# Kernel tuning notes

Hardware: AMD Instinct MI355X
Metric: run time of the kernel (lower is better)

Reference implementation:

```python
import jax, jax.numpy as jnp
import numpy as np

B, T, D = 8, 2048, 1024   # batch, seq_len (== block_size), n_embed
HS = 128                   # head_size

def setup_inputs() -> dict:
    key = jax.random.key(0)
    kx, kk, kq, kv = jax.random.split(key, 4)
    s = D ** -0.5  # torch Linear default init scale ~ U(-1/sqrt(in), 1/sqrt(in))
    x  = jax.random.normal(kx, (B, T, D), dtype=jnp.float32)
    Wk = jax.random.uniform(kk, (HS, D), jnp.float32, -s, s)
    Wq = jax.random.uniform(kq, (HS, D), jnp.float32, -s, s)
    Wv = jax.random.uniform(kv, (HS, D), jnp.float32, -s, s)
    return {"x": x, "Wk": Wk, "Wq": Wq, "Wv": Wv}

def reference(x, Wk, Wq, Wv):
    # single-head causal self-attention; dropout disabled (eval mode)
    Tlen = x.shape[1]
    k = jnp.einsum('btd,hd->bth', x, Wk)   # [B,T,HS]
    q = jnp.einsum('btd,hd->bth', x, Wq)
    v = jnp.einsum('btd,hd->bth', x, Wv)
    scale = Wk.shape[0] ** -0.5
    scores = jnp.einsum('bth,bsh->bts', q, k) * scale   # [B,T,T]
    causal = jnp.tril(jnp.ones((Tlen, Tlen), dtype=bool))
    scores = jnp.where(causal, scores, -jnp.inf)
    weights = jax.nn.softmax(scores, axis=-1)
    out = jnp.einsum('bts,bsh->bth', weights, v)        # [B,T,HS]
    return out
```

## Files before the change

kernel.cpp:

```cpp
#include <hip/hip_runtime.h>
#include <hip/hip_bf16.h>
#include <math.h>

#define BATCH_N 8
#define SEQ_T   2048
#define DIM_D   1024
#define HS_N    128

using bf16x8_t = __attribute__((ext_vector_type(8))) __bf16;
using bf16x4_t = __attribute__((ext_vector_type(4))) __bf16;
using f32x4_t  = __attribute__((ext_vector_type(4))) float;

__device__ __forceinline__ f32x4_t mfma_16x16x32(bf16x8_t a, bf16x8_t b, f32x4_t c) {
  return __builtin_amdgcn_mfma_f32_16x16x32_bf16(a, b, c, 0, 0, 0);
}

__device__ __forceinline__ void async_cp16(const void* g, void* l) {
  __builtin_amdgcn_global_load_lds(
      (const __attribute__((address_space(1))) unsigned int*)g,
      (__attribute__((address_space(3))) unsigned int*)l, 16, 0, 0);
}

#define BAR()      __builtin_amdgcn_s_barrier()
#define FENCE()    asm volatile("" ::: "memory")
#define WAIT_VM(n) asm volatile("s_waitcnt vmcnt(" #n ")" ::: "memory")
#define WAIT_LGKM0 asm volatile("s_waitcnt lgkmcnt(0)" ::: "memory")

__global__ __launch_bounds__(256) void castw_kernel(
    const float* __restrict__ Wk, const float* __restrict__ Wq,
    const float* __restrict__ Wv, __bf16* __restrict__ Wb,
    unsigned int* __restrict__ km) {
  if (blockIdx.x == 0 && threadIdx.x < 8) km[threadIdx.x] = 0u;
  int idx = blockIdx.x * 256 + threadIdx.x;
  int e   = idx * 4;
  int row = e >> 10;
  int col = e & 1023;
  const float* src;
  float sc = 1.0f;
  if (row < 128) {
    src = Wk + row * DIM_D + col;
  } else if (row < 256) {
    src = Wq + (row - 128) * DIM_D + col;
    sc  = 0.08838834764831845f;
  } else {
    src = Wv + (row - 256) * DIM_D + col;
  }
  float4 v = *(const float4*)src;
  bf16x4_t o;
  o[0] = (__bf16)(v.x * sc); o[1] = (__bf16)(v.y * sc);
  o[2] = (__bf16)(v.z * sc); o[3] = (__bf16)(v.w * sc);
  *(bf16x4_t*)(Wb + e) = o;
}

__global__ __launch_bounds__(256, 2) void proj_kernel(
    const float* __restrict__ x, const __bf16* __restrict__ Wb,
    __bf16* __restrict__ Qb, __bf16* __restrict__ Kb, __bf16* __restrict__ Vt) {
  __shared__ __align__(16) char psmem[81920];
  __bf16* A = (__bf16*)psmem;

  const int tid  = threadIdx.x;
  const int lane = tid & 63;
  const int wave = tid >> 6;
  const int lr = lane & 15;
  const int lq = lane >> 4;
  const int m0 = blockIdx.x * 32;

  f32x4_t acc[2][6];
  #pragma unroll
  for (int mt = 0; mt < 2; ++mt)
    #pragma unroll
    for (int nt = 0; nt < 6; ++nt) acc[mt][nt] = (f32x4_t){0.f, 0.f, 0.f, 0.f};

  auto stageB = [&](int bufi, int kt) {
    __bf16* Bs = (__bf16*)(psmem + 32768 + bufi * 24576);
    for (int c = wave; c < 24; c += 4) {
      const int row = c * 16 + (lane >> 2);
      const int u   = (lane & 3) ^ ((row >> 1) & 3);
      async_cp16(Wb + (size_t)row * DIM_D + kt * 32 + u * 8, Bs + c * 512);
    }
  };

  stageB(0, 0);

  for (int p = 0; p < 2; ++p) {
    __syncthreads();

    {
      const int r  = tid >> 3;
      const int t  = tid & 7;
      const float* xs = x + (size_t)(m0 + r) * DIM_D + p * 512;
      __bf16* as = A + r * 512;
      const int sw = r & 7;
      #pragma unroll
      for (int i = 0; i < 8; ++i) {
        const int u = t + 8 * i;
        float4 f0 = *(const float4*)(xs + u * 8);
        float4 f1 = *(const float4*)(xs + u * 8 + 4);
        bf16x8_t a;
        a[0] = (__bf16)f0.x; a[1] = (__bf16)f0.y;
        a[2] = (__bf16)f0.z; a[3] = (__bf16)f0.w;
        a[4] = (__bf16)f1.x; a[5] = (__bf16)f1.y;
        a[6] = (__bf16)f1.z; a[7] = (__bf16)f1.w;
        *(bf16x8_t*)(as + ((u ^ sw) * 8)) = a;
      }
    }
    __syncthreads();

    for (int kt2 = 0; kt2 < 16; ++kt2) {
      const int kt  = p * 16 + kt2;
      const int cur = kt & 1;
      if (kt + 1 < 32) {
        stageB(cur ^ 1, kt + 1);
        WAIT_VM(6);
      } else {
        WAIT_VM(0);
      }
      BAR();
      FENCE();
      const __bf16* Bs = (const __bf16*)(psmem + 32768 + cur * 24576);

      bf16x8_t af[2];
      #pragma unroll
      for (int mt = 0; mt < 2; ++mt) {
        const int ml = mt * 16 + lr;
        const int u  = kt2 * 4 + lq;
        af[mt] = *(const bf16x8_t*)(&A[ml * 512 + ((u ^ (ml & 7)) * 8)]);
      }
      bf16x8_t bfv[6];
      #pragma unroll
      for (int nt = 0; nt < 6; ++nt) {
        const int nl = wave * 96 + nt * 16 + lr;
        bfv[nt] = *(const bf16x8_t*)(&Bs[nl * 32 + ((lq ^ ((nl >> 1) & 3)) * 8)]);
      }
      #pragma unroll
      for (int mt = 0; mt < 2; ++mt)
        #pragma unroll
        for (int nt = 0; nt < 6; ++nt)
          acc[mt][nt] = mfma_16x16x32(af[mt], bfv[nt], acc[mt][nt]);
      WAIT_LGKM0;
      BAR();
      FENCE();
    }
  }

  #pragma unroll
  for (int mt = 0; mt < 2; ++mt) {
    const int t0 = m0 + mt * 16 + lq * 4;
    #pragma unroll
    for (int nt = 0; nt < 6; ++nt) {
      const int nn = wave * 96 + nt * 16 + lr;
      if (nn < 256) {
        __bf16* dst = (nn < 128) ? (Kb + nn) : (Qb + (nn - 128));
        #pragma unroll
        for (int r = 0; r < 4; ++r)
          dst[(size_t)(t0 + r) * HS_N] = (__bf16)acc[mt][nt][r];
      } else {
        const int bb = t0 >> 11;
        const int tl = t0 & 2047;
        bf16x4_t o;
        #pragma unroll
        for (int r = 0; r < 4; ++r) o[r] = (__bf16)acc[mt][nt][r];
        *(bf16x4_t*)(Vt + (size_t)bb * (HS_N * SEQ_T) + (size_t)(nn - 256) * SEQ_T + tl) = o;
      }
    }
  }
}

__global__ __launch_bounds__(256) void knorm_kernel(
    const __bf16* __restrict__ Kb, unsigned int* __restrict__ km) {
  const int t = blockIdx.x * 256 + threadIdx.x;
  const __bf16* kp = Kb + (size_t)t * HS_N;
  float ss = 0.f;
  #pragma unroll
  for (int i = 0; i < 16; ++i) {
    bf16x8_t v = *(const bf16x8_t*)(kp + i * 8);
    #pragma unroll
    for (int j = 0; j < 8; ++j) { float f = (float)v[j]; ss += f * f; }
  }
  #pragma unroll
  for (int off = 1; off < 64; off <<= 1) ss = fmaxf(ss, __shfl_xor(ss, off));
  if ((threadIdx.x & 63) == 0) atomicMax(km + (t >> 11), __float_as_uint(ss));
}

__global__ __launch_bounds__(256, 2) void attn_kernel(
    const __bf16* __restrict__ Qb, const __bf16* __restrict__ Kb,
    const __bf16* __restrict__ Vt, const unsigned int* __restrict__ km,
    __bf16* __restrict__ Opart, float* __restrict__ lpart) {
  __shared__ __align__(16) char smem[81920];
  __bf16* KsBase = (__bf16*)smem;
  __bf16* VsBase = (__bf16*)(smem + 32768);
  float*  Ofl    = (float*)smem;

  const int lane = threadIdx.x & 63;
  const int wave = threadIdx.x >> 6;
  const int lr = lane & 15;
  const int lq = lane >> 4;
  const int bid  = blockIdx.x;
  const int b    = bid & 7;
  const int rest = bid >> 3;
  const int jg   = 15 - (rest >> 2);
  const int p4   = rest & 3;
  const int Q0   = jg * 128;
  const int qa   = Q0 + wave * 32;
  const int ch   = 2 * (jg + 1);
  const int c0   = (p4 * ch) >> 2;
  const int c1   = ((p4 + 1) * ch) >> 2;

  const __bf16* Qbb = Qb + (size_t)b * (SEQ_T * HS_N);
  const __bf16* Kbb = Kb + (size_t)b * (SEQ_T * HS_N);
  const __bf16* Vbb = Vt + (size_t)b * (HS_N * SEQ_T);
  __bf16* pbA = (__bf16*)(smem + 65536 + wave * 4096);
  __bf16* pbB = (__bf16*)(smem + 65536 + wave * 4096 + 2048);

  bf16x8_t qf[2][4];
  #pragma unroll
  for (int t = 0; t < 2; ++t)
    #pragma unroll
    for (int ks = 0; ks < 4; ++ks)
      qf[t][ks] = *(const bf16x8_t*)(Qbb + (size_t)(qa + t * 16 + lr) * HS_N
                                     + ks * 32 + lq * 8);

  const float km2 = __uint_as_float(km[b]);
  float mrow[2][4];
  #pragma unroll
  for (int t = 0; t < 2; ++t) {
    float qn2 = 0.f;
    #pragma unroll
    for (int ks = 0; ks < 4; ++ks)
      #pragma unroll
      for (int j = 0; j < 8; ++j) { float f = (float)qf[t][ks][j]; qn2 += f * f; }
    qn2 += __shfl_xor(qn2, 16);
    qn2 += __shfl_xor(qn2, 32);
    #pragma unroll
    for (int r2 = 0; r2 < 4; ++r2)
      mrow[t][r2] = sqrtf(__shfl(qn2, lq * 4 + r2) * km2);
  }

  f32x4_t Oa[2][8];
  #pragma unroll
  for (int t = 0; t < 2; ++t)
    #pragma unroll
    for (int o = 0; o < 8; ++o) Oa[t][o] = (f32x4_t){0.f, 0.f, 0.f, 0.f};
  float lsum[2][4] = {{0.f,0.f,0.f,0.f},{0.f,0.f,0.f,0.f}};

  auto stage = [&](int bufi, int c) {
    const int kk = c * 64;
    __bf16* Ks = KsBase + bufi * 8192;
    for (int idx = wave; idx < 32; idx += 4) {
      if (idx < 16) {
        const int row = idx * 4 + (lane >> 4);
        const int u   = (lane & 15) ^ (row & 15);
        async_cp16(Kbb + (size_t)(kk + row) * HS_N + u * 8, Ks + idx * 512);
      } else {
        const int i2  = idx - 16;
        const int row = i2 * 8 + (lane >> 3);
        const int u   = (lane & 7) ^ (row & 7);
        async_cp16(Vbb + (size_t)row * SEQ_T + kk + u * 8, VsBase + bufi * 8192 + i2 * 512);
      }
    }
  };

  if (c0 < c1) stage(0, c0);
  __syncthreads();

  for (int c = c0; c < c1; ++c) {
    const int cur = (c - c0) & 1;
    if (c + 1 < c1) {
      stage(cur ^ 1, c + 1);
      WAIT_VM(8);
    } else {
      WAIT_VM(0);
    }
    BAR();
    FENCE();

    const int kk = c * 64;
    const __bf16* Ks = KsBase + cur * 8192;
    const __bf16* Vs = VsBase + cur * 8192;

    f32x4_t s0[4], s1[4];
    #pragma unroll
    for (int nt = 0; nt < 4; ++nt) {
      s0[nt] = (f32x4_t){0.f, 0.f, 0.f, 0.f};
      s1[nt] = (f32x4_t){0.f, 0.f, 0.f, 0.f};
    }
    #pragma unroll
    for (int ks = 0; ks < 4; ++ks)
      #pragma unroll
      for (int nt = 0; nt < 4; ++nt) {
        bf16x8_t kf = *(const bf16x8_t*)(
            &Ks[(nt * 16 + lr) * 128 + (((ks * 4 + lq) ^ lr) * 8)]);
        s0[nt] = mfma_16x16x32(qf[0][ks], kf, s0[nt]);
        s1[nt] = mfma_16x16x32(qf[1][ks], kf, s1[nt]);
      }
    const int q0a = qa, q0b = qa + 16;
    if (kk + 63 > q0a) {
      #pragma unroll
      for (int nt = 0; nt < 4; ++nt) {
        const int col = kk + nt * 16 + lr;
        #pragma unroll
        for (int r2 = 0; r2 < 4; ++r2)
          if (col > q0a + lq * 4 + r2) s0[nt][r2] = -INFINITY;
      }
    }
    if (kk + 63 > q0b) {
      #pragma unroll
      for (int nt = 0; nt < 4; ++nt) {
        const int col = kk + nt * 16 + lr;
        #pragma unroll
        for (int r2 = 0; r2 < 4; ++r2)
          if (col > q0b + lq * 4 + r2) s1[nt][r2] = -INFINITY;
      }
    }

    #pragma unroll
    for (int r2 = 0; r2 < 4; ++r2) {
      float a0 = __expf(s0[0][r2] - mrow[0][r2]);
      float a1 = __expf(s0[1][r2] - mrow[0][r2]);
      float a2 = __expf(s0[2][r2] - mrow[0][r2]);
      float a3 = __expf(s0[3][r2] - mrow[0][r2]);
      s0[0][r2] = a0; s0[1][r2] = a1; s0[2][r2] = a2; s0[3][r2] = a3;
      lsum[0][r2] += (a0 + a1) + (a2 + a3);
      float b0 = __expf(s1[0][r2] - mrow[1][r2]);
      float b1 = __expf(s1[1][r2] - mrow[1][r2]);
      float b2 = __expf(s1[2][r2] - mrow[1][r2]);
      float b3 = __expf(s1[3][r2] - mrow[1][r2]);
      s1[0][r2] = b0; s1[1][r2] = b1; s1[2][r2] = b2; s1[3][r2] = b3;
      lsum[1][r2] += (b0 + b1) + (b2 + b3);
    }

    #pragma unroll
    for (int nt = 0; nt < 4; ++nt)
      #pragma unroll
      for (int r2 = 0; r2 < 4; ++r2) {
        const int prow = lq * 4 + r2;
        const int pcol = (nt * 16 + lr) ^ ((prow & 7) << 3);
        pbA[prow * 64 + pcol] = (__bf16)s0[nt][r2];
        pbB[prow * 64 + pcol] = (__bf16)s1[nt][r2];
      }

    #pragma unroll
    for (int k2 = 0; k2 < 2; ++k2) {
      const int au = ((k2 * 4 + lq) ^ (lr & 7)) << 3;
      bf16x8_t afrA = *(const bf16x8_t*)(pbA + lr * 64 + au);
      bf16x8_t afrB = *(const bf16x8_t*)(pbB + lr * 64 + au);
      #pragma unroll
      for (int o = 0; o < 8; ++o) {
        bf16x8_t vfr = *(const bf16x8_t*)(
            &Vs[(o * 16 + lr) * 64 + (((k2 * 4 + lq) ^ (lr & 7)) * 8)]);
        Oa[0][o] = mfma_16x16x32(afrA, vfr, Oa[0][o]);
        Oa[1][o] = mfma_16x16x32(afrB, vfr, Oa[1][o]);
      }
    }
    WAIT_LGKM0;
    BAR();
    FENCE();
  }

  #pragma unroll
  for (int t = 0; t < 2; ++t)
    #pragma unroll
    for (int r2 = 0; r2 < 4; ++r2) {
      float v = lsum[t][r2];
      v += __shfl_xor(v, 1);
      v += __shfl_xor(v, 2);
      v += __shfl_xor(v, 4);
      v += __shfl_xor(v, 8);
      if (lr == 0)
        lpart[bid * 128 + wave * 32 + t * 16 + lq * 4 + r2] = v;
    }

  #pragma unroll
  for (int t = 0; t < 2; ++t)
    #pragma unroll
    for (int o = 0; o < 8; ++o)
      #pragma unroll
      for (int r2 = 0; r2 < 4; ++r2)
        Ofl[(wave * 32 + t * 16 + lq * 4 + r2) * 132 + o * 16 + lr] = Oa[t][o][r2];
  __syncthreads();

  {
    const int row = threadIdx.x >> 1;
    const int cb  = (threadIdx.x & 1) * 64;
    __bf16* dst = Opart + ((size_t)bid * 128 + row) * 128 + cb;
    #pragma unroll
    for (int g2 = 0; g2 < 16; ++g2) {
      float4 f = *(const float4*)(&Ofl[row * 132 + cb + g2 * 4]);
      bf16x4_t o;
      o[0] = (__bf16)f.x; o[1] = (__bf16)f.y; o[2] = (__bf16)f.z; o[3] = (__bf16)f.w;
      *(bf16x4_t*)(dst + g2 * 4) = o;
    }
  }
}

__global__ __launch_bounds__(256) void merge_kernel(
    const __bf16* __restrict__ Opart, const float* __restrict__ lpart,
    float* __restrict__ out) {
  const int idx = blockIdx.x * 256 + threadIdx.x;
  const int row = idx >> 5;
  const int c4  = (idx & 31) * 4;
  const int b   = row >> 11;
  const int tl  = row & 2047;
  const int jg  = tl >> 7;
  const int lrow = tl & 127;
  const int rbase = (15 - jg) * 4;
  float a0 = 0.f, a1 = 0.f, a2 = 0.f, a3 = 0.f, l = 0.f;
  #pragma unroll
  for (int p = 0; p < 4; ++p) {
    const int s = b + 8 * (rbase + p);
    bf16x4_t a = *(const bf16x4_t*)(Opart + ((size_t)s * 128 + lrow) * 128 + c4);
    a0 += (float)a[0]; a1 += (float)a[1]; a2 += (float)a[2]; a3 += (float)a[3];
    l += lpart[s * 128 + lrow];
  }
  const float inv = 1.0f / l;
  float4 o;
  o.x = a0 * inv; o.y = a1 * inv; o.z = a2 * inv; o.w = a3 * inv;
  *(float4*)(out + (size_t)row * HS_N + c4) = o;
}

extern "C" void kernel_launch(void* const* d_in, const int* in_sizes, int n_in,
                              void* d_out, int out_size, void* d_ws, size_t ws_size,
                              hipStream_t stream) {
  const float* x  = (const float*)d_in[0];
  const float* Wk = (const float*)d_in[1];
  const float* Wq = (const float*)d_in[2];
  const float* Wv = (const float*)d_in[3];
  float* out = (float*)d_out;

  char* ws = (char*)d_ws;
  __bf16* Wb = (__bf16*)ws;
  __bf16* Qb = (__bf16*)(ws + 786432);
  __bf16* Kb = (__bf16*)(ws + 786432 + 4194304);
  __bf16* Vt = (__bf16*)(ws + 786432 + 8388608);
  unsigned int* km = (unsigned int*)(ws + 13369344);
  __bf16* Opart = (__bf16*)(ws + 13369600);
  float*  lpart = (float*)(ws + 30146816);

  castw_kernel<<<384, 256, 0, stream>>>(Wk, Wq, Wv, Wb, km);
  proj_kernel<<<512, 256, 0, stream>>>(x, Wb, Qb, Kb, Vt);
  knorm_kernel<<<64, 256, 0, stream>>>(Kb, km);
  attn_kernel<<<512, 256, 0, stream>>>(Qb, Kb, Vt, km, Opart, lpart);
  merge_kernel<<<2048, 256, 0, stream>>>(Opart, lpart, out);
}
```

Before: 163.4 us.

## Load projection weights directly into registers with 3-stage prefetch, drop LDS staging

The projection kernel no longer stages weight tiles through LDS with async copies and per-iteration barriers. Each wave now loads its weight fragments straight from global memory into registers through a 3-deep rotating prefetch, so the main loop has no barriers. The whole 32x1024 activation tile is converted to bf16 in LDS once, up front. This removes barrier and LDS traffic but leaves weight loads uncoalesced (strided rows per lane) and adds register pressure that may hurt occupancy.

```diff
diff --git a/kernel.cpp b/kernel.cpp
--- a/kernel.cpp
+++ b/kernel.cpp
@@ -55,8 +55,7 @@
 __global__ __launch_bounds__(256, 2) void proj_kernel(
     const float* __restrict__ x, const __bf16* __restrict__ Wb,
     __bf16* __restrict__ Qb, __bf16* __restrict__ Kb, __bf16* __restrict__ Vt) {
-  __shared__ __align__(16) char psmem[81920];
-  __bf16* A = (__bf16*)psmem;
+  __shared__ __align__(16) __bf16 A[32 * 1024];
 
   const int tid  = threadIdx.x;
   const int lane = tid & 63;
@@ -71,76 +70,70 @@
     #pragma unroll
     for (int nt = 0; nt < 6; ++nt) acc[mt][nt] = (f32x4_t){0.f, 0.f, 0.f, 0.f};
 
-  auto stageB = [&](int bufi, int kt) {
-    __bf16* Bs = (__bf16*)(psmem + 32768 + bufi * 24576);
-    for (int c = wave; c < 24; c += 4) {
-      const int row = c * 16 + (lane >> 2);
-      const int u   = (lane & 3) ^ ((row >> 1) & 3);
-      async_cp16(Wb + (size_t)row * DIM_D + kt * 32 + u * 8, Bs + c * 512);
-    }
-  };
-
-  stageB(0, 0);
-
-  for (int p = 0; p < 2; ++p) {
-    __syncthreads();
-
-    {
-      const int r  = tid >> 3;
-      const int t  = tid & 7;
-      const float* xs = x + (size_t)(m0 + r) * DIM_D + p * 512;
-      __bf16* as = A + r * 512;
-      const int sw = r & 7;
-      #pragma unroll
-      for (int i = 0; i < 8; ++i) {
-        const int u = t + 8 * i;
-        float4 f0 = *(const float4*)(xs + u * 8);
-        float4 f1 = *(const float4*)(xs + u * 8 + 4);
-        bf16x8_t a;
-        a[0] = (__bf16)f0.x; a[1] = (__bf16)f0.y;
-        a[2] = (__bf16)f0.z; a[3] = (__bf16)f0.w;
-        a[4] = (__bf16)f1.x; a[5] = (__bf16)f1.y;
-        a[6] = (__bf16)f1.z; a[7] = (__bf16)f1.w;
-        *(bf16x8_t*)(as + ((u ^ sw) * 8)) = a;
-      }
-    }
-    __syncthreads();
-
-    for (int kt2 = 0; kt2 < 16; ++kt2) {
-      const int kt  = p * 16 + kt2;
-      const int cur = kt & 1;
-      if (kt + 1 < 32) {
-        stageB(cur ^ 1, kt + 1);
-        WAIT_VM(6);
-      } else {
-        WAIT_VM(0);
-      }
-      BAR();
-      FENCE();
-      const __bf16* Bs = (const __bf16*)(psmem + 32768 + cur * 24576);
-
-      bf16x8_t af[2];
+  const __bf16* bp[6];
+  #pragma unroll
+  for (int nt = 0; nt < 6; ++nt)
+    bp[nt] = Wb + (size_t)(wave * 96 + nt * 16 + lr) * DIM_D + lq * 8;
+
+  bf16x8_t bq[3][6];
+  bf16x8_t aq[3][2];
+
+  #pragma unroll
+  for (int s = 0; s < 2; ++s)
+    #pragma unroll
+    for (int nt = 0; nt < 6; ++nt)
+      bq[s][nt] = *(const bf16x8_t*)(bp[nt] + s * 32);
+
+  {
+    const int r  = tid >> 3;
+    const int t  = tid & 7;
+    const float* xs = x + (size_t)(m0 + r) * DIM_D;
+    __bf16* as = A + r * 1024;
+    const int sw = r & 7;
+    #pragma unroll
+    for (int i = 0; i < 16; ++i) {
+      const int u = t + 8 * i;
+      float4 f0 = *(const float4*)(xs + u * 8);
+      float4 f1 = *(const float4*)(xs + u * 8 + 4);
+      bf16x8_t a;
+      a[0] = (__bf16)f0.x; a[1] = (__bf16)f0.y;
+      a[2] = (__bf16)f0.z; a[3] = (__bf16)f0.w;
+      a[4] = (__bf16)f1.x; a[5] = (__bf16)f1.y;
+      a[6] = (__bf16)f1.z; a[7] = (__bf16)f1.w;
+      *(bf16x8_t*)(as + ((u ^ sw) * 8)) = a;
+    }
+  }
+  __syncthreads();
+
+  #pragma unroll
+  for (int s = 0; s < 2; ++s)
+    #pragma unroll
+    for (int mt = 0; mt < 2; ++mt) {
+      const int ml = mt * 16 + lr;
+      const int u  = s * 4 + lq;
+      aq[s][mt] = *(const bf16x8_t*)(&A[ml * 1024 + ((u ^ (ml & 7)) * 8)]);
+    }
+
+  #pragma unroll
+  for (int kt = 0; kt < 32; ++kt) {
+    const int cs = kt % 3;
+    if (kt + 2 < 32) {
+      const int ns = (kt + 2) % 3;
+      #pragma unroll
+      for (int nt = 0; nt < 6; ++nt)
+        bq[ns][nt] = *(const bf16x8_t*)(bp[nt] + (kt + 2) * 32);
       #pragma unroll
       for (int mt = 0; mt < 2; ++mt) {
         const int ml = mt * 16 + lr;
-        const int u  = kt2 * 4 + lq;
-        af[mt] = *(const bf16x8_t*)(&A[ml * 512 + ((u ^ (ml & 7)) * 8)]);
-      }
-      bf16x8_t bfv[6];
-      #pragma unroll
-      for (int nt = 0; nt < 6; ++nt) {
-        const int nl = wave * 96 + nt * 16 + lr;
-        bfv[nt] = *(const bf16x8_t*)(&Bs[nl * 32 + ((lq ^ ((nl >> 1) & 3)) * 8)]);
-      }
-      #pragma unroll
-      for (int mt = 0; mt < 2; ++mt)
-        #pragma unroll
-        for (int nt = 0; nt < 6; ++nt)
-          acc[mt][nt] = mfma_16x16x32(af[mt], bfv[nt], acc[mt][nt]);
-      WAIT_LGKM0;
-      BAR();
-      FENCE();
-    }
+        const int u  = (kt + 2) * 4 + lq;
+        aq[ns][mt] = *(const bf16x8_t*)(&A[ml * 1024 + ((u ^ (ml & 7)) * 8)]);
+      }
+    }
+    #pragma unroll
+    for (int mt = 0; mt < 2; ++mt)
+      #pragma unroll
+      for (int nt = 0; nt < 6; ++nt)
+        acc[mt][nt] = mfma_16x16x32(aq[cs][mt], bq[cs][nt], acc[mt][nt]);
   }
 
   #pragma unroll
```

Measured after the change: 181.0 us. 1.11x slower.
